# Performance work log

Measured on AMD Instinct MI355X. Metric: run time of the kernel, lower is better.

Reference implementation:

```python
import jax, jax.numpy as jnp
import numpy as np

B, N, E, H = 2, 2048, 1024, 16
D = E // H  # head_dim = 64


def setup_inputs() -> dict:
    key = jax.random.key(0)
    ks = jax.random.split(key, 8)
    s = 1.0 / np.sqrt(D)
    return {
        "query": jax.random.normal(ks[0], (B, N, E), jnp.float32),
        "key": jax.random.normal(ks[1], (B, N, E), jnp.float32),
        "value": jax.random.normal(ks[2], (B, N, E), jnp.float32),
        "mask": jax.random.randint(ks[3], (B, N), 0, 2, jnp.int32),
        # per-head Linear weights, torch layout (out_features, in_features) stacked over heads
        "Wq": jax.random.uniform(ks[4], (H, D, D), jnp.float32, -s, s),
        "Wk": jax.random.uniform(ks[5], (H, D, D), jnp.float32, -s, s),
        "Wv": jax.random.uniform(ks[6], (H, D, D), jnp.float32, -s, s),
        "Wo": jax.random.uniform(ks[7], (E, E), jnp.float32, -1.0 / np.sqrt(E), 1.0 / np.sqrt(E)),
    }


def reference(query, key, value, mask, Wq, Wk, Wv, Wo):
    b, n, e = query.shape
    h, d, _ = Wq.shape
    q = query.reshape(b, n, h, d)
    k = key.reshape(b, n, h, d)
    v = value.reshape(b, n, h, d)
    # per-head Linear (no bias): x @ W[i].T, batched over heads
    qh = jnp.einsum('bnhd,hed->bnhe', q, Wq)
    kh = jnp.einsum('bnhd,hed->bnhe', k, Wk)
    vh = jnp.einsum('bnhd,hed->bnhe', v, Wv)
    # NOTE: original scales by sqrt(embed_size), not sqrt(head_dim)
    scores = jnp.einsum('bqhd,bkhd->bhqk', qh, kh) / (e ** 0.5)
    # NOTE: mask is unsqueezed on the KEY axis position in torch (dim=2),
    # so it masks entire QUERY rows, broadcasting over keys.
    scores = jnp.where(mask[:, None, :, None] == 0, jnp.float32(-1e28), scores)
    probs = jax.nn.softmax(scores, axis=-1)
    attn = jnp.einsum('bhqk,bkhd->bqhd', probs, vh).reshape(b, n, e)
    return attn @ Wo.T
```

## Files before the change

kernel.cpp:

```cpp
#include <hip/hip_runtime.h>
#include <hip/hip_bf16.h>

#define B_ 2
#define N_ 2048
#define E_ 1024
#define H_ 16
#define D_ 64
#define BH_ (B_ * H_)

typedef __attribute__((ext_vector_type(4))) float f32x4;
typedef __attribute__((ext_vector_type(8))) short bf16x8;
typedef __attribute__((ext_vector_type(4))) short s16x4;
typedef __attribute__((ext_vector_type(4))) int i32x4;
typedef __attribute__((ext_vector_type(2))) int i32x2;
typedef __attribute__((ext_vector_type(4))) _Float16 f16x4;

#define MFMA(a, b, c) __builtin_amdgcn_mfma_f32_16x16x32_bf16(a, b, c, 0, 0, 0)
#define MFMA16(a, b, c) __builtin_amdgcn_mfma_f32_16x16x16f16(a, b, c, 0, 0, 0)

#define AS1(p) ((const __attribute__((address_space(1))) unsigned int*)(p))
#define AS3(p) ((__attribute__((address_space(3))) unsigned int*)(p))

static __device__ __forceinline__ unsigned short f2bf(float f) {
    unsigned int u = __builtin_bit_cast(unsigned int, f);
    u += 0x7fff + ((u >> 16) & 1);
    return (unsigned short)(u >> 16);
}
static __device__ __forceinline__ int pack2bf(float lo, float hi) {
    __hip_bfloat162 t = __float22bfloat162_rn(float2{lo, hi});
    int r;
    __builtin_memcpy(&r, &t, 4);
    return r;
}
static __device__ __forceinline__ bf16x8 cvt8s(const float* __restrict__ p, float sc) {
    f32x4 a = *(const f32x4*)p;
    f32x4 b = *(const f32x4*)(p + 4);
    i32x4 r = {pack2bf(a.x * sc, a.y * sc), pack2bf(a.z * sc, a.w * sc),
               pack2bf(b.x * sc, b.y * sc), pack2bf(b.z * sc, b.w * sc)};
    return __builtin_bit_cast(bf16x8, r);
}
static __device__ __forceinline__ f16x4 pack4f16(f32x4 p) {
    auto lo = __builtin_amdgcn_cvt_pkrtz(p.x, p.y);
    auto hi = __builtin_amdgcn_cvt_pkrtz(p.z, p.w);
    f16x4 r;
    __builtin_memcpy(&r, &lo, 4);
    __builtin_memcpy(((char*)&r) + 4, &hi, 4);
    return r;
}

__global__ __launch_bounds__(256, 4)
void proj_kernel(const float* __restrict__ q, const float* __restrict__ k,
                 const float* __restrict__ v,
                 const float* __restrict__ Wq, const float* __restrict__ Wk,
                 const float* __restrict__ Wv,
                 const int* __restrict__ mask,
                 unsigned short* __restrict__ qh, unsigned short* __restrict__ kh,
                 unsigned short* __restrict__ vt) {
    const int z = blockIdx.z;
    const float* X = (z == 0) ? q : (z == 1) ? k : v;
    const float* W = (z == 0) ? Wq : (z == 1) ? Wk : Wv;
    unsigned short* out = (z == 0) ? qh : (z == 1) ? kh : vt;
    const float wscale = (z == 0) ? (1.44269504f * 0.03125f) : 1.0f;

    const int lane = threadIdx.x & 63;
    const int wave = threadIdx.x >> 6;
    const int l16  = lane & 15;
    const int quad = lane >> 4;
    const int bh = blockIdx.y;
    const int b = bh >> 4, h = bh & 15;
    const int n0 = blockIdx.x * 64;
    const int tok = n0 + wave * 16 + l16;

    const float* xrow = X + ((size_t)(b * N_ + tok)) * E_ + h * 64;
    bf16x8 xf[2];
    xf[0] = cvt8s(xrow + quad * 8, 1.0f);
    xf[1] = cvt8s(xrow + 32 + quad * 8, 1.0f);

    const float* Wh = W + (size_t)h * 64 * 64;
    bf16x8 wf[4][2];
#pragma unroll
    for (int t4 = 0; t4 < 4; ++t4) {
        const float* wrow = Wh + (t4 * 16 + l16) * 64;
        wf[t4][0] = cvt8s(wrow + quad * 8, wscale);
        wf[t4][1] = cvt8s(wrow + 32 + quad * 8, wscale);
    }

    const int mk = (z == 0) ? mask[b * N_ + tok] : 1;

#pragma unroll
    for (int mi = 0; mi < 4; ++mi) {
        f32x4 a = {0.f, 0.f, 0.f, 0.f};
        a = MFMA(wf[mi][0], xf[0], a);
        a = MFMA(wf[mi][1], xf[1], a);
        if (z != 2) {
            i32x2 pk = {pack2bf(a.x, a.y), pack2bf(a.z, a.w)};
            if (!mk) pk = (i32x2){0, 0};
            *(i32x2*)(out + ((size_t)bh * N_ + tok) * 64 + mi * 16 + quad * 4) = pk;
        } else {
#pragma unroll
            for (int r = 0; r < 4; ++r) {
                int dout = mi * 16 + quad * 4 + r;
                _Float16 hv = (_Float16)a[r];
                unsigned short us;
                __builtin_memcpy(&us, &hv, 2);
                out[((size_t)bh * 64 + dout) * N_ + tok] = us;
            }
        }
    }
}

__global__ __launch_bounds__(256)
void cvt_wo_kernel(const float* __restrict__ wo, unsigned short* __restrict__ wob) {
    int idx = blockIdx.x * 256 + threadIdx.x;
    f32x4 v = *(const f32x4*)(wo + (size_t)idx * 4);
    i32x2 r = {pack2bf(v.x, v.y), pack2bf(v.z, v.w)};
    *(i32x2*)(wob + (size_t)idx * 4) = r;
}

__global__ __launch_bounds__(256, 2)
void attn_kernel(const unsigned short* __restrict__ qh,
                 const unsigned short* __restrict__ kh,
                 const unsigned short* __restrict__ vt,
                 unsigned short* __restrict__ attnb) {
    __shared__ short Kb[2][64 * 72];
    __shared__ short Vb[3][64 * 76];

    const int tid  = threadIdx.x;
    const int lane = tid & 63;
    const int wave = tid >> 6;
    const int l16  = lane & 15;
    const int quad = lane >> 4;

    const int flat = blockIdx.y * gridDim.x + blockIdx.x;
    const int qblk = flat >> 5;
    const int rem  = flat & 31;
    const int bh   = ((rem & 7) << 2) | (rem >> 3);
    const int b = bh >> 4, h = bh & 15;
    const int q0 = qblk * 128 + wave * 32;

    const unsigned short* kbase = kh + (size_t)bh * N_ * 64;
    const unsigned short* vbase = vt + (size_t)bh * 64 * N_;

    const int c0i = tid;
    const int c1i = tid + 256;
    const int k0o = (c0i >> 3) * 72 + (c0i & 7) * 8;
    const int k1o = (c1i >> 3) * 72 + (c1i & 7) * 8;
    const int v0o = (c0i >> 3) * 76 + (c0i & 7) * 8;
    const int v1o = (c1i >> 3) * 76 + (c1i & 7) * 8;

    short* kcur  = &Kb[0][0];
    short* knext = &Kb[1][0];
    short* vprev = &Vb[2][0];
    short* vcur  = &Vb[0][0];
    short* vnext = &Vb[1][0];

    bf16x8 qf[2][2];
#pragma unroll
    for (int qi = 0; qi < 2; ++qi) {
        const unsigned short* qrow = qh + ((size_t)bh * N_ + q0 + qi * 16 + l16) * 64;
        qf[qi][0] = *(const bf16x8*)(qrow + quad * 8);
        qf[qi][1] = *(const bf16x8*)(qrow + 32 + quad * 8);
    }

    f32x4 psum[2] = {{0.f, 0.f, 0.f, 0.f}, {0.f, 0.f, 0.f, 0.f}};
    f32x4 o[4][2];
#pragma unroll
    for (int mi = 0; mi < 4; ++mi)
#pragma unroll
        for (int qi = 0; qi < 2; ++qi) o[mi][qi] = (f32x4){0.f, 0.f, 0.f, 0.f};

    f16x4 pf[2][4];

    bf16x8 gK0, gK1, gV0, gV1;
    gK0 = *(const bf16x8*)(kbase + c0i * 8);
    gK1 = *(const bf16x8*)(kbase + c1i * 8);
    gV0 = *(const bf16x8*)(vbase + (size_t)(c0i >> 3) * N_ + (c0i & 7) * 8);
    gV1 = *(const bf16x8*)(vbase + (size_t)(c1i >> 3) * N_ + (c1i & 7) * 8);
    *(bf16x8*)(kcur + k0o) = gK0;
    *(bf16x8*)(kcur + k1o) = gK1;
    *(bf16x8*)(vcur + v0o) = gV0;
    *(bf16x8*)(vcur + v1o) = gV1;
    __syncthreads();

    for (int kt = 0; kt < N_ / 64; ++kt) {
        if (kt + 1 < N_ / 64) {
            const int k0n = (kt + 1) * 64;
            gK0 = *(const bf16x8*)(kbase + (size_t)k0n * 64 + c0i * 8);
            gK1 = *(const bf16x8*)(kbase + (size_t)k0n * 64 + c1i * 8);
            gV0 = *(const bf16x8*)(vbase + (size_t)(c0i >> 3) * N_ + k0n + (c0i & 7) * 8);
            gV1 = *(const bf16x8*)(vbase + (size_t)(c1i >> 3) * N_ + k0n + (c1i & 7) * 8);
        }

        bf16x8 ka[4][2];
#pragma unroll
        for (int t4 = 0; t4 < 4; ++t4) {
            ka[t4][0] = *(const bf16x8*)(kcur + (t4 * 16 + l16) * 72 + quad * 8);
            ka[t4][1] = *(const bf16x8*)(kcur + (t4 * 16 + l16) * 72 + 32 + quad * 8);
        }
        f32x4 s[2][4];
#pragma unroll
        for (int qi = 0; qi < 2; ++qi)
#pragma unroll
            for (int t4 = 0; t4 < 4; ++t4) {
                f32x4 z = {0.f, 0.f, 0.f, 0.f};
                z = MFMA(ka[t4][0], qf[qi][0], z);
                z = MFMA(ka[t4][1], qf[qi][1], z);
                s[qi][t4] = z;
            }

        if (kt > 0) {
#pragma unroll
            for (int mi = 0; mi < 4; ++mi) {
#pragma unroll
                for (int t4 = 0; t4 < 4; ++t4) {
                    f16x4 va = *(const f16x4*)(vprev + (mi * 16 + l16) * 76 +
                                               t4 * 16 + quad * 4);
#pragma unroll
                    for (int qi = 0; qi < 2; ++qi)
                        o[mi][qi] = MFMA16(va, pf[qi][t4], o[mi][qi]);
                }
            }
        }

#pragma unroll
        for (int qi = 0; qi < 2; ++qi) {
#pragma unroll
            for (int t4 = 0; t4 < 4; ++t4) {
                f32x4 p;
#pragma unroll
                for (int r = 0; r < 4; ++r) p[r] = __builtin_amdgcn_exp2f(s[qi][t4][r]);
                psum[qi] += p;
                pf[qi][t4] = pack4f16(p);
            }
        }

        if (kt + 1 < N_ / 64) {
            *(bf16x8*)(knext + k0o) = gK0;
            *(bf16x8*)(knext + k1o) = gK1;
            *(bf16x8*)(vnext + v0o) = gV0;
            *(bf16x8*)(vnext + v1o) = gV1;
            __syncthreads();
        }

        short* t = kcur; kcur = knext; knext = t;
        short* tv = vprev; vprev = vcur; vcur = vnext; vnext = tv;
    }

#pragma unroll
    for (int mi = 0; mi < 4; ++mi) {
#pragma unroll
        for (int t4 = 0; t4 < 4; ++t4) {
            f16x4 va = *(const f16x4*)(vprev + (mi * 16 + l16) * 76 +
                                       t4 * 16 + quad * 4);
#pragma unroll
            for (int qi = 0; qi < 2; ++qi)
                o[mi][qi] = MFMA16(va, pf[qi][t4], o[mi][qi]);
        }
    }

#pragma unroll
    for (int qi = 0; qi < 2; ++qi) {
        float rs = psum[qi].x + psum[qi].y + psum[qi].z + psum[qi].w;
        rs += __shfl_xor(rs, 16);
        rs += __shfl_xor(rs, 32);
        const float inv = 1.0f / rs;
        const int qrow_idx = q0 + qi * 16 + l16;
#pragma unroll
        for (int mi = 0; mi < 4; ++mi) {
            f32x4 ov = o[mi][qi];
            i32x2 pkk = {pack2bf(ov.x * inv, ov.y * inv),
                         pack2bf(ov.z * inv, ov.w * inv)};
            int d0 = mi * 16 + quad * 4;
            *(i32x2*)(attnb + ((size_t)(b * N_ + qrow_idx)) * E_ + h * 64 + d0) = pkk;
        }
    }
}

__global__ __launch_bounds__(512, 1)
void out_gemm_kernel(const unsigned short* __restrict__ A,
                     const unsigned short* __restrict__ Bw,
                     float* __restrict__ out) {
    __shared__ short As[2][128 * 32];
    __shared__ short Bs[2][128 * 32];

    const int tid  = threadIdx.x;
    const int lane = tid & 63;
    const int l16  = lane & 15;
    const int quad = lane >> 4;
    const int wave = tid >> 6;
    const int wm = wave & 1, wn = wave >> 1;
    const int m0 = blockIdx.x * 128;
    const int n0 = blockIdx.y * 128;

    const unsigned short* gA = A + (size_t)m0 * E_;
    const unsigned short* gB = Bw + (size_t)n0 * E_;

    f32x4 acc[4][2];
#pragma unroll
    for (int mt = 0; mt < 4; ++mt)
#pragma unroll
        for (int nt = 0; nt < 2; ++nt) acc[mt][nt] = (f32x4){0.f, 0.f, 0.f, 0.f};

    const int cc = tid >> 7, rr = tid & 127;
#define OG_STAGE(buf, k0)                                                        \
    {                                                                            \
        __builtin_amdgcn_global_load_lds(AS1(gA + (size_t)rr * E_ + (k0) + cc * 8), \
                                         AS3(&As[buf][tid * 8]), 16, 0, 0);      \
        __builtin_amdgcn_global_load_lds(AS1(gB + (size_t)rr * E_ + (k0) + cc * 8), \
                                         AS3(&Bs[buf][tid * 8]), 16, 0, 0);      \
    }

    OG_STAGE(0, 0)
    __syncthreads();

    for (int kt = 0; kt < E_ / 32; ++kt) {
        const int cur = kt & 1;
        if (kt + 1 < E_ / 32) OG_STAGE(cur ^ 1, (kt + 1) * 32)

        bf16x8 af[4], bf[2];
#pragma unroll
        for (int mt = 0; mt < 4; ++mt)
            af[mt] = *(const bf16x8*)(&As[cur][(quad * 128 + wm * 64 + mt * 16 + l16) * 8]);
#pragma unroll
        for (int nt = 0; nt < 2; ++nt)
            bf[nt] = *(const bf16x8*)(&Bs[cur][(quad * 128 + wn * 32 + nt * 16 + l16) * 8]);

#pragma unroll
        for (int mt = 0; mt < 4; ++mt)
#pragma unroll
            for (int nt = 0; nt < 2; ++nt)
                acc[mt][nt] = MFMA(af[mt], bf[nt], acc[mt][nt]);

        __syncthreads();
    }

#pragma unroll
    for (int mt = 0; mt < 4; ++mt)
#pragma unroll
        for (int nt = 0; nt < 2; ++nt)
#pragma unroll
            for (int r = 0; r < 4; ++r)
                out[(size_t)(m0 + wm * 64 + mt * 16 + quad * 4 + r) * E_ +
                    n0 + wn * 32 + nt * 16 + l16] = acc[mt][nt][r];
#undef OG_STAGE
}

extern "C" void kernel_launch(void* const* d_in, const int* in_sizes, int n_in,
                              void* d_out, int out_size, void* d_ws, size_t ws_size,
                              hipStream_t stream) {
    const float* q    = (const float*)d_in[0];
    const float* k    = (const float*)d_in[1];
    const float* v    = (const float*)d_in[2];
    const int*   mask = (const int*)d_in[3];
    const float* Wq   = (const float*)d_in[4];
    const float* Wk   = (const float*)d_in[5];
    const float* Wv   = (const float*)d_in[6];
    const float* Wo   = (const float*)d_in[7];
    float* out = (float*)d_out;

    char* ws = (char*)d_ws;
    unsigned short* qh    = (unsigned short*)(ws);
    unsigned short* kh    = (unsigned short*)(ws + (size_t)8 * 1024 * 1024);
    unsigned short* vt    = (unsigned short*)(ws + (size_t)16 * 1024 * 1024);
    unsigned short* attnb = (unsigned short*)(ws + (size_t)24 * 1024 * 1024);
    unsigned short* wob   = (unsigned short*)(ws);

    dim3 blk(256);
    proj_kernel<<<dim3(N_ / 64, BH_, 3), blk, 0, stream>>>(q, k, v, Wq, Wk, Wv, mask,
                                                           qh, kh, vt);
    attn_kernel<<<dim3(16, 32), blk, 0, stream>>>(qh, kh, vt, attnb);
    cvt_wo_kernel<<<dim3(E_ * E_ / 1024), blk, 0, stream>>>(Wo, wob);
    out_gemm_kernel<<<dim3(32, 8), dim3(512), 0, stream>>>(attnb, wob, out);
}
```

Baseline: 200.0 us.

## Pre-tile Q/K/V layouts and stream K/V tiles via direct global-to-LDS loads

The projection kernel now writes Q/K/V in a tiled, MFMA-fragment-friendly layout, so each 64-token tile is contiguous and can be copied straight into LDS. The attention kernel uses global_load_lds to stage K and V asynchronously, which removes the register round-trip and the padded LDS layout. It also shrinks blocks to 128 threads over 64 query rows with double buffers and adds s_setprio around the MFMA sections. The cost is a single barrier per tile with less latency hiding per block, and the loop is hand-unrolled through a macro.

New measurement: 215.1 us. 7.5% more time.

```diff
diff --git a/kernel.cpp b/kernel.cpp
--- a/kernel.cpp
+++ b/kernel.cpp
@@ -7,10 +7,10 @@
 #define H_ 16
 #define D_ 64
 #define BH_ (B_ * H_)
+#define NT_ (N_ / 64)
 
 typedef __attribute__((ext_vector_type(4))) float f32x4;
 typedef __attribute__((ext_vector_type(8))) short bf16x8;
-typedef __attribute__((ext_vector_type(4))) short s16x4;
 typedef __attribute__((ext_vector_type(4))) int i32x4;
 typedef __attribute__((ext_vector_type(2))) int i32x2;
 typedef __attribute__((ext_vector_type(4))) _Float16 f16x4;
@@ -21,11 +21,6 @@
 #define AS1(p) ((const __attribute__((address_space(1))) unsigned int*)(p))
 #define AS3(p) ((__attribute__((address_space(3))) unsigned int*)(p))
 
-static __device__ __forceinline__ unsigned short f2bf(float f) {
-    unsigned int u = __builtin_bit_cast(unsigned int, f);
-    u += 0x7fff + ((u >> 16) & 1);
-    return (unsigned short)(u >> 16);
-}
 static __device__ __forceinline__ int pack2bf(float lo, float hi) {
     __hip_bfloat162 t = __float22bfloat162_rn(float2{lo, hi});
     int r;
@@ -69,7 +64,8 @@
     const int bh = blockIdx.y;
     const int b = bh >> 4, h = bh & 15;
     const int n0 = blockIdx.x * 64;
-    const int tok = n0 + wave * 16 + l16;
+    const int row = wave * 16 + l16;
+    const int tok = n0 + row;
 
     const float* xrow = X + ((size_t)(b * N_ + tok)) * E_ + h * 64;
     bf16x8 xf[2];
@@ -86,6 +82,7 @@
     }
 
     const int mk = (z == 0) ? mask[b * N_ + tok] : 1;
+    unsigned short* tbase = out + ((size_t)bh * N_ + n0) * 64;
 
 #pragma unroll
     for (int mi = 0; mi < 4; ++mi) {
@@ -95,7 +92,8 @@
         if (z != 2) {
             i32x2 pk = {pack2bf(a.x, a.y), pack2bf(a.z, a.w)};
             if (!mk) pk = (i32x2){0, 0};
-            *(i32x2*)(out + ((size_t)bh * N_ + tok) * 64 + mi * 16 + quad * 4) = pk;
+            *(i32x2*)(tbase + ((mi * 2 + (quad >> 1)) * 64 + row) * 8 +
+                      (quad & 1) * 4) = pk;
         } else {
 #pragma unroll
             for (int r = 0; r < 4; ++r) {
@@ -103,7 +101,7 @@
                 _Float16 hv = (_Float16)a[r];
                 unsigned short us;
                 __builtin_memcpy(&us, &hv, 2);
-                out[((size_t)bh * 64 + dout) * N_ + tok] = us;
+                tbase[((row >> 2) * 64 + dout) * 4 + (row & 3)] = us;
             }
         }
     }
@@ -117,13 +115,13 @@
     *(i32x2*)(wob + (size_t)idx * 4) = r;
 }
 
-__global__ __launch_bounds__(256, 2)
+__global__ __launch_bounds__(128, 2)
 void attn_kernel(const unsigned short* __restrict__ qh,
                  const unsigned short* __restrict__ kh,
                  const unsigned short* __restrict__ vt,
                  unsigned short* __restrict__ attnb) {
-    __shared__ short Kb[2][64 * 72];
-    __shared__ short Vb[3][64 * 76];
+    __shared__ short Kb[2][4096];
+    __shared__ short Vb[2][4096];
 
     const int tid  = threadIdx.x;
     const int lane = tid & 63;
@@ -136,31 +134,19 @@
     const int rem  = flat & 31;
     const int bh   = ((rem & 7) << 2) | (rem >> 3);
     const int b = bh >> 4, h = bh & 15;
-    const int q0 = qblk * 128 + wave * 32;
+    const int q0 = qblk * 64 + wave * 32;
 
     const unsigned short* kbase = kh + (size_t)bh * N_ * 64;
-    const unsigned short* vbase = vt + (size_t)bh * 64 * N_;
-
-    const int c0i = tid;
-    const int c1i = tid + 256;
-    const int k0o = (c0i >> 3) * 72 + (c0i & 7) * 8;
-    const int k1o = (c1i >> 3) * 72 + (c1i & 7) * 8;
-    const int v0o = (c0i >> 3) * 76 + (c0i & 7) * 8;
-    const int v1o = (c1i >> 3) * 76 + (c1i & 7) * 8;
-
-    short* kcur  = &Kb[0][0];
-    short* knext = &Kb[1][0];
-    short* vprev = &Vb[2][0];
-    short* vcur  = &Vb[0][0];
-    short* vnext = &Vb[1][0];
+    const unsigned short* vbase = vt + (size_t)bh * N_ * 64;
+    const unsigned short* qtile = qh + ((size_t)bh * N_ + qblk * 64) * 64;
 
     bf16x8 qf[2][2];
 #pragma unroll
-    for (int qi = 0; qi < 2; ++qi) {
-        const unsigned short* qrow = qh + ((size_t)bh * N_ + q0 + qi * 16 + l16) * 64;
-        qf[qi][0] = *(const bf16x8*)(qrow + quad * 8);
-        qf[qi][1] = *(const bf16x8*)(qrow + 32 + quad * 8);
-    }
+    for (int qi = 0; qi < 2; ++qi)
+#pragma unroll
+        for (int half = 0; half < 2; ++half)
+            qf[qi][half] = *(const bf16x8*)(qtile +
+                ((half * 4 + quad) * 64 + wave * 32 + qi * 16 + l16) * 8);
 
     f32x4 psum[2] = {{0.f, 0.f, 0.f, 0.f}, {0.f, 0.f, 0.f, 0.f}};
     f32x4 o[4][2];
@@ -171,92 +157,94 @@
 
     f16x4 pf[2][4];
 
-    bf16x8 gK0, gK1, gV0, gV1;
-    gK0 = *(const bf16x8*)(kbase + c0i * 8);
-    gK1 = *(const bf16x8*)(kbase + c1i * 8);
-    gV0 = *(const bf16x8*)(vbase + (size_t)(c0i >> 3) * N_ + (c0i & 7) * 8);
-    gV1 = *(const bf16x8*)(vbase + (size_t)(c1i >> 3) * N_ + (c1i & 7) * 8);
-    *(bf16x8*)(kcur + k0o) = gK0;
-    *(bf16x8*)(kcur + k1o) = gK1;
-    *(bf16x8*)(vcur + v0o) = gV0;
-    *(bf16x8*)(vcur + v1o) = gV1;
+#pragma unroll
+    for (int i = 0; i < 4; ++i)
+        __builtin_amdgcn_global_load_lds(AS1(kbase + tid * 8 + i * 1024),
+                                         AS3(&Kb[0][tid * 8 + i * 1024]), 16, 0, 0);
     __syncthreads();
 
-    for (int kt = 0; kt < N_ / 64; ++kt) {
-        if (kt + 1 < N_ / 64) {
-            const int k0n = (kt + 1) * 64;
-            gK0 = *(const bf16x8*)(kbase + (size_t)k0n * 64 + c0i * 8);
-            gK1 = *(const bf16x8*)(kbase + (size_t)k0n * 64 + c1i * 8);
-            gV0 = *(const bf16x8*)(vbase + (size_t)(c0i >> 3) * N_ + k0n + (c0i & 7) * 8);
-            gV1 = *(const bf16x8*)(vbase + (size_t)(c1i >> 3) * N_ + k0n + (c1i & 7) * 8);
-        }
-
-        bf16x8 ka[4][2];
+#define BODY(T, CUR, DO_PV, DO_STAGEK)                                           \
+    {                                                                            \
+        if (DO_STAGEK) {                                                         \
+            const unsigned short* ksrc = kbase + (size_t)((T) + 1) * 4096;       \
+            _Pragma("unroll")                                                    \
+            for (int i = 0; i < 4; ++i)                                          \
+                __builtin_amdgcn_global_load_lds(                                \
+                    AS1(ksrc + tid * 8 + i * 1024),                              \
+                    AS3(&Kb[(CUR) ^ 1][tid * 8 + i * 1024]), 16, 0, 0);          \
+        }                                                                        \
+        {                                                                        \
+            const unsigned short* vsrc = vbase + (size_t)(T) * 4096;             \
+            _Pragma("unroll")                                                    \
+            for (int i = 0; i < 4; ++i)                                          \
+                __builtin_amdgcn_global_load_lds(                                \
+                    AS1(vsrc + tid * 8 + i * 1024),                              \
+                    AS3(&Vb[CUR][tid * 8 + i * 1024]), 16, 0, 0);                \
+        }                                                                        \
+        __builtin_amdgcn_s_setprio(1);                                           \
+        f32x4 s[2][4];                                                           \
+        _Pragma("unroll")                                                        \
+        for (int t4 = 0; t4 < 4; ++t4) {                                         \
+            bf16x8 ka0 = *(const bf16x8*)(&Kb[CUR][((0 * 4 + quad) * 64 +        \
+                                                    t4 * 16 + l16) * 8]);        \
+            bf16x8 ka1 = *(const bf16x8*)(&Kb[CUR][((1 * 4 + quad) * 64 +        \
+                                                    t4 * 16 + l16) * 8]);        \
+            _Pragma("unroll")                                                    \
+            for (int qi = 0; qi < 2; ++qi) {                                     \
+                f32x4 zz = {0.f, 0.f, 0.f, 0.f};                                 \
+                zz = MFMA(ka0, qf[qi][0], zz);                                   \
+                zz = MFMA(ka1, qf[qi][1], zz);                                   \
+                s[qi][t4] = zz;                                                  \
+            }                                                                    \
+        }                                                                        \
+        if (DO_PV) {                                                             \
+            _Pragma("unroll")                                                    \
+            for (int mi = 0; mi < 4; ++mi) {                                     \
+                _Pragma("unroll")                                                \
+                for (int t4 = 0; t4 < 4; ++t4) {                                 \
+                    f16x4 va = *(const f16x4*)(&Vb[(CUR) ^ 1][                   \
+                        ((t4 * 4 + quad) * 64 + mi * 16 + l16) * 4]);            \
+                    _Pragma("unroll")                                            \
+                    for (int qi = 0; qi < 2; ++qi)                               \
+                        o[mi][qi] = MFMA16(va, pf[qi][t4], o[mi][qi]);           \
+                }                                                                \
+            }                                                                    \
+        }                                                                        \
+        __builtin_amdgcn_s_setprio(0);                                           \
+        _Pragma("unroll")                                                        \
+        for (int qi = 0; qi < 2; ++qi) {                                         \
+            _Pragma("unroll")                                                    \
+            for (int t4 = 0; t4 < 4; ++t4) {                                     \
+                f32x4 p;                                                         \
+                _Pragma("unroll")                                                \
+                for (int r = 0; r < 4; ++r)                                      \
+                    p[r] = __builtin_amdgcn_exp2f(s[qi][t4][r]);                 \
+                psum[qi] += p;                                                   \
+                pf[qi][t4] = pack4f16(p);                                        \
+            }                                                                    \
+        }                                                                        \
+        __syncthreads();                                                         \
+    }
+
+    BODY(0, 0, 0, 1)
+    for (int t = 1; t < NT_ - 1; t += 2) {
+        BODY(t, 1, 1, 1)
+        BODY(t + 1, 0, 1, 1)
+    }
+    BODY(NT_ - 1, 1, 1, 0)
+
+#pragma unroll
+    for (int mi = 0; mi < 4; ++mi) {
 #pragma unroll
         for (int t4 = 0; t4 < 4; ++t4) {
-            ka[t4][0] = *(const bf16x8*)(kcur + (t4 * 16 + l16) * 72 + quad * 8);
-            ka[t4][1] = *(const bf16x8*)(kcur + (t4 * 16 + l16) * 72 + 32 + quad * 8);
-        }
-        f32x4 s[2][4];
-#pragma unroll
-        for (int qi = 0; qi < 2; ++qi)
-#pragma unroll
-            for (int t4 = 0; t4 < 4; ++t4) {
-                f32x4 z = {0.f, 0.f, 0.f, 0.f};
-                z = MFMA(ka[t4][0], qf[qi][0], z);
-                z = MFMA(ka[t4][1], qf[qi][1], z);
-                s[qi][t4] = z;
-            }
-
-        if (kt > 0) {
-#pragma unroll
-            for (int mi = 0; mi < 4; ++mi) {
-#pragma unroll
-                for (int t4 = 0; t4 < 4; ++t4) {
-                    f16x4 va = *(const f16x4*)(vprev + (mi * 16 + l16) * 76 +
-                                               t4 * 16 + quad * 4);
-#pragma unroll
-                    for (int qi = 0; qi < 2; ++qi)
-                        o[mi][qi] = MFMA16(va, pf[qi][t4], o[mi][qi]);
-                }
-            }
-        }
-
-#pragma unroll
-        for (int qi = 0; qi < 2; ++qi) {
-#pragma unroll
-            for (int t4 = 0; t4 < 4; ++t4) {
-                f32x4 p;
-#pragma unroll
-                for (int r = 0; r < 4; ++r) p[r] = __builtin_amdgcn_exp2f(s[qi][t4][r]);
-                psum[qi] += p;
-                pf[qi][t4] = pack4f16(p);
-            }
-        }
-
-        if (kt + 1 < N_ / 64) {
-            *(bf16x8*)(knext + k0o) = gK0;
-            *(bf16x8*)(knext + k1o) = gK1;
-            *(bf16x8*)(vnext + v0o) = gV0;
-            *(bf16x8*)(vnext + v1o) = gV1;
-            __syncthreads();
-        }
-
-        short* t = kcur; kcur = knext; knext = t;
-        short* tv = vprev; vprev = vcur; vcur = vnext; vnext = tv;
-    }
-
-#pragma unroll
-    for (int mi = 0; mi < 4; ++mi) {
-#pragma unroll
-        for (int t4 = 0; t4 < 4; ++t4) {
-            f16x4 va = *(const f16x4*)(vprev + (mi * 16 + l16) * 76 +
-                                       t4 * 16 + quad * 4);
+            f16x4 va = *(const f16x4*)(&Vb[1][((t4 * 4 + quad) * 64 +
+                                               mi * 16 + l16) * 4]);
 #pragma unroll
             for (int qi = 0; qi < 2; ++qi)
                 o[mi][qi] = MFMA16(va, pf[qi][t4], o[mi][qi]);
         }
     }
+#undef BODY
 
 #pragma unroll
     for (int qi = 0; qi < 2; ++qi) {
@@ -365,10 +353,9 @@
     unsigned short* attnb = (unsigned short*)(ws + (size_t)24 * 1024 * 1024);
     unsigned short* wob   = (unsigned short*)(ws);
 
-    dim3 blk(256);
-    proj_kernel<<<dim3(N_ / 64, BH_, 3), blk, 0, stream>>>(q, k, v, Wq, Wk, Wv, mask,
-                                                           qh, kh, vt);
-    attn_kernel<<<dim3(16, 32), blk, 0, stream>>>(qh, kh, vt, attnb);
-    cvt_wo_kernel<<<dim3(E_ * E_ / 1024), blk, 0, stream>>>(Wo, wob);
+    proj_kernel<<<dim3(N_ / 64, BH_, 3), dim3(256), 0, stream>>>(q, k, v, Wq, Wk, Wv,
+                                                                 mask, qh, kh, vt);
+    attn_kernel<<<dim3(32, 32), dim3(128), 0, stream>>>(qh, kh, vt, attnb);
+    cvt_wo_kernel<<<dim3(E_ * E_ / 1024), dim3(256), 0, stream>>>(Wo, wob);
     out_gemm_kernel<<<dim3(32, 8), dim3(512), 0, stream>>>(attnb, wob, out);
 }
```

## Retile output GEMM to 64x128 with K=64 stages and add MFMA priority hints

Applied to the files above, without the earlier changes.

The output projection GEMM now uses 64x128 tiles with a 64-wide K step, launching twice as many blocks (512 vs 256) with occupancy hint 4, which halves the number of K iterations and barriers. The 256-CU device should then be better filled. s_setprio raises wave priority around the MFMA sections in both the attention and GEMM kernels so the matrix work gets issued ahead of other waves. An unused f2bf helper is removed. Smaller tiles mean less reuse of each loaded element, and more LDS per block is used.

Measured after the change: 203.0 us. About the same (+1.5%).

```diff
diff --git a/kernel.cpp b/kernel.cpp
--- a/kernel.cpp
+++ b/kernel.cpp
@@ -21,11 +21,6 @@
 #define AS1(p) ((const __attribute__((address_space(1))) unsigned int*)(p))
 #define AS3(p) ((__attribute__((address_space(3))) unsigned int*)(p))
 
-static __device__ __forceinline__ unsigned short f2bf(float f) {
-    unsigned int u = __builtin_bit_cast(unsigned int, f);
-    u += 0x7fff + ((u >> 16) & 1);
-    return (unsigned short)(u >> 16);
-}
 static __device__ __forceinline__ int pack2bf(float lo, float hi) {
     __hip_bfloat162 t = __float22bfloat162_rn(float2{lo, hi});
     int r;
@@ -191,6 +186,7 @@
             gV1 = *(const bf16x8*)(vbase + (size_t)(c1i >> 3) * N_ + k0n + (c1i & 7) * 8);
         }
 
+        __builtin_amdgcn_s_setprio(1);
         bf16x8 ka[4][2];
 #pragma unroll
         for (int t4 = 0; t4 < 4; ++t4) {
@@ -221,6 +217,7 @@
                 }
             }
         }
+        __builtin_amdgcn_s_setprio(0);
 
 #pragma unroll
         for (int qi = 0; qi < 2; ++qi) {
@@ -246,6 +243,7 @@
         short* tv = vprev; vprev = vcur; vcur = vnext; vnext = tv;
     }
 
+    __builtin_amdgcn_s_setprio(1);
 #pragma unroll
     for (int mi = 0; mi < 4; ++mi) {
 #pragma unroll
@@ -257,6 +255,7 @@
                 o[mi][qi] = MFMA16(va, pf[qi][t4], o[mi][qi]);
         }
     }
+    __builtin_amdgcn_s_setprio(0);
 
 #pragma unroll
     for (int qi = 0; qi < 2; ++qi) {
@@ -276,71 +275,82 @@
     }
 }
 
-__global__ __launch_bounds__(512, 1)
+__global__ __launch_bounds__(512, 4)
 void out_gemm_kernel(const unsigned short* __restrict__ A,
                      const unsigned short* __restrict__ Bw,
                      float* __restrict__ out) {
-    __shared__ short As[2][128 * 32];
-    __shared__ short Bs[2][128 * 32];
+    __shared__ short As[2][64 * 64];
+    __shared__ short Bs[2][128 * 64];
 
     const int tid  = threadIdx.x;
     const int lane = tid & 63;
     const int l16  = lane & 15;
     const int quad = lane >> 4;
     const int wave = tid >> 6;
-    const int wm = wave & 1, wn = wave >> 1;
-    const int m0 = blockIdx.x * 128;
+    const int wm = wave >> 2;
+    const int wn = wave & 3;
+    const int m0 = blockIdx.x * 64;
     const int n0 = blockIdx.y * 128;
 
     const unsigned short* gA = A + (size_t)m0 * E_;
     const unsigned short* gB = Bw + (size_t)n0 * E_;
 
-    f32x4 acc[4][2];
-#pragma unroll
-    for (int mt = 0; mt < 4; ++mt)
+    f32x4 acc[2][2];
+#pragma unroll
+    for (int mt = 0; mt < 2; ++mt)
 #pragma unroll
         for (int nt = 0; nt < 2; ++nt) acc[mt][nt] = (f32x4){0.f, 0.f, 0.f, 0.f};
 
-    const int cc = tid >> 7, rr = tid & 127;
-#define OG_STAGE(buf, k0)                                                        \
-    {                                                                            \
-        __builtin_amdgcn_global_load_lds(AS1(gA + (size_t)rr * E_ + (k0) + cc * 8), \
-                                         AS3(&As[buf][tid * 8]), 16, 0, 0);      \
-        __builtin_amdgcn_global_load_lds(AS1(gB + (size_t)rr * E_ + (k0) + cc * 8), \
-                                         AS3(&Bs[buf][tid * 8]), 16, 0, 0);      \
+#define OG_STAGE(buf, k0)                                                          \
+    {                                                                              \
+        __builtin_amdgcn_global_load_lds(                                          \
+            AS1(gA + (size_t)(tid & 63) * E_ + (k0) + (tid >> 6) * 8),             \
+            AS3(&As[buf][tid * 8]), 16, 0, 0);                                     \
+        __builtin_amdgcn_global_load_lds(                                          \
+            AS1(gB + (size_t)(tid & 127) * E_ + (k0) + (tid >> 7) * 8),            \
+            AS3(&Bs[buf][tid * 8]), 16, 0, 0);                                     \
+        __builtin_amdgcn_global_load_lds(                                          \
+            AS1(gB + (size_t)(tid & 127) * E_ + (k0) + ((tid + 512) >> 7) * 8),    \
+            AS3(&Bs[buf][(tid + 512) * 8]), 16, 0, 0);                             \
     }
 
     OG_STAGE(0, 0)
     __syncthreads();
 
-    for (int kt = 0; kt < E_ / 32; ++kt) {
+    for (int kt = 0; kt < E_ / 64; ++kt) {
         const int cur = kt & 1;
-        if (kt + 1 < E_ / 32) OG_STAGE(cur ^ 1, (kt + 1) * 32)
-
-        bf16x8 af[4], bf[2];
-#pragma unroll
-        for (int mt = 0; mt < 4; ++mt)
-            af[mt] = *(const bf16x8*)(&As[cur][(quad * 128 + wm * 64 + mt * 16 + l16) * 8]);
+        if (kt + 1 < E_ / 64) OG_STAGE(cur ^ 1, (kt + 1) * 64)
+
+        __builtin_amdgcn_s_setprio(1);
+#pragma unroll
+        for (int kh = 0; kh < 2; ++kh) {
+            bf16x8 af[2], bf[2];
+#pragma unroll
+            for (int mt = 0; mt < 2; ++mt)
+                af[mt] = *(const bf16x8*)(&As[cur][((kh * 4 + quad) * 64 +
+                                                    wm * 32 + mt * 16 + l16) * 8]);
+#pragma unroll
+            for (int nt = 0; nt < 2; ++nt)
+                bf[nt] = *(const bf16x8*)(&Bs[cur][((kh * 4 + quad) * 128 +
+                                                    wn * 32 + nt * 16 + l16) * 8]);
+#pragma unroll
+            for (int mt = 0; mt < 2; ++mt)
+#pragma unroll
+                for (int nt = 0; nt < 2; ++nt)
+                    acc[mt][nt] = MFMA(af[mt], bf[nt], acc[mt][nt]);
+        }
+        __builtin_amdgcn_s_setprio(0);
+
+        __syncthreads();
+    }
+
+#pragma unroll
+    for (int mt = 0; mt < 2; ++mt)
 #pragma unroll
         for (int nt = 0; nt < 2; ++nt)
-            bf[nt] = *(const bf16x8*)(&Bs[cur][(quad * 128 + wn * 32 + nt * 16 + l16) * 8]);
-
-#pragma unroll
-        for (int mt = 0; mt < 4; ++mt)
-#pragma unroll
-            for (int nt = 0; nt < 2; ++nt)
-                acc[mt][nt] = MFMA(af[mt], bf[nt], acc[mt][nt]);
-
-        __syncthreads();
-    }
-
-#pragma unroll
-    for (int mt = 0; mt < 4; ++mt)
-#pragma unroll
-        for (int nt = 0; nt < 2; ++nt)
 #pragma unroll
             for (int r = 0; r < 4; ++r)
-                out[(size_t)(m0 + wm * 64 + mt * 16 + quad * 4 + r) * E_ +
+                out[(size_t)(m0 + wm * 32 + mt * 16 + quad * 4 + r) * E_ +
                     n0 + wn * 32 + nt * 16 + l16] = acc[mt][nt][r];
 #undef OG_STAGE
 }
@@ -370,5 +380,5 @@
                                                            qh, kh, vt);
     attn_kernel<<<dim3(16, 32), blk, 0, stream>>>(qh, kh, vt, attnb);
     cvt_wo_kernel<<<dim3(E_ * E_ / 1024), blk, 0, stream>>>(Wo, wob);
-    out_gemm_kernel<<<dim3(32, 8), dim3(512), 0, stream>>>(attnb, wob, out);
-}
+    out_gemm_kernel<<<dim3(64, 8), dim3(512), 0, stream>>>(attnb, wob, out);
+}
```
